# Kernel tuning notes

Hardware: AMD Instinct MI355X
Metric: run time of the kernel (lower is better)

## Reference

```python
import jax, jax.numpy as jnp
import numpy as np

# Grid / model constants (apt_original_dims = (B,H,W,T,BS,D))
B, H, W, T, BS, D = 8, 32, 32, 4, 3, 768
SMAX = 2  # apt_num_scales=2 -> patch sizes in {1, 2}


def _make_positions():
    """Tile each (H,W) grid per timestep with 2x2 blocks; exactly half the
    blocks become one coarse size-2 patch, the rest four size-1 patches.
    Returns int32 [B, P, 4] with rows (y, x, size, t); P identical per sample."""
    rng = np.random.default_rng(0)
    blocks = [(by, bx, t) for t in range(T) for by in range(H // SMAX) for bx in range(W // SMAX)]
    n_blocks = len(blocks)
    pos_all = []
    for b in range(B):
        coarse = rng.permutation(n_blocks) < n_blocks // 2
        plist = []
        for (by, bx, t), c in zip(blocks, coarse):
            y, x = by * SMAX, bx * SMAX
            if c:
                plist.append((y, x, SMAX, t))
            else:
                for dy in range(SMAX):
                    for dx in range(SMAX):
                        plist.append((y + dy, x + dx, 1, t))
        pos_all.append(plist)
    return np.asarray(pos_all, dtype=np.int32)  # [B, P, 4]


def setup_inputs() -> dict:
    key = jax.random.key(0)
    positions = jnp.asarray(_make_positions())            # [B, P, 4]
    P = positions.shape[1]                                # 2560
    modality_tokens = jax.random.normal(key, (B, P * BS, D), dtype=jnp.float32)
    return {"modality_tokens": modality_tokens, "positions": positions}


def reference(modality_tokens, positions):
    """Faithful jax version of split_and_expand_per_modality for the APT
    modality: scatter patch tokens to [B,H,W,T,BS,D], broadcasting coarse
    (size>1) tokens over the s x s grid cells they cover.
    Vectorized as: build a cell->patch-id map via one scatter, then gather."""
    Bn, P, _ = positions.shape
    y, x, size, t = positions[..., 0], positions[..., 1], positions[..., 2], positions[..., 3]

    # All offsets inside a max-size patch footprint: [SMAX*SMAX]
    dy, dx = jnp.meshgrid(jnp.arange(SMAX), jnp.arange(SMAX), indexing='ij')
    dy, dx = dy.reshape(-1), dx.reshape(-1)

    yy = y[:, :, None] + dy[None, None, :]                # [B, P, S2]
    xx = x[:, :, None] + dx[None, None, :]
    valid = (dy[None, None, :] < size[:, :, None]) & (dx[None, None, :] < size[:, :, None])

    flat = (yy * W + xx) * T + t[:, :, None]              # flat cell index
    flat = jnp.where(valid, flat, H * W * T)              # invalid -> dummy slot

    pid = jnp.broadcast_to(jnp.arange(P, dtype=jnp.int32)[None, :, None], flat.shape)
    b_idx = jnp.broadcast_to(jnp.arange(Bn)[:, None, None], flat.shape)

    id_map = jnp.full((Bn, H * W * T + 1), -1, dtype=jnp.int32)
    id_map = id_map.at[b_idx, flat].set(pid)              # cell -> covering patch id
    id_map = id_map[:, : H * W * T].reshape(Bn, H, W, T)

    tok = modality_tokens.reshape(Bn, P, BS, D)

    def gather_one(tok_b, idm_b):
        out = tok_b[jnp.maximum(idm_b, 0)]                # [H, W, T, BS, D]
        return jnp.where((idm_b >= 0)[..., None, None], out, jnp.zeros((), tok_b.dtype))

    return jax.vmap(gather_one)(tok, id_map)              # [B, H, W, T, BS, D]
```

## Files before the change

### kernel.cpp

```cpp
#include <hip/hip_runtime.h>


constexpr int H_ = 32;
constexpr int W_ = 32;
constexpr int T_ = 4;
constexpr int BS_ = 3;
constexpr int D_ = 768;
constexpr int CD  = BS_ * D_;
constexpr int CD4 = CD / 4;
constexpr int BLOCK = 192;
constexpr int BN_ = 8;
constexpr int CELLS = BN_ * H_ * W_ * T_;
constexpr int NXCD = 8;

typedef float f4 __attribute__((ext_vector_type(4)));

__global__ __launch_bounds__(256) void build_map_kernel(
    const int4* __restrict__ pos,
    int* __restrict__ map,
    int P)
{
    const int bp = blockIdx.x * 256 + threadIdx.x;
    if (bp >= BN_ * P) return;
    const int b = bp / P;
    const int4 q = pos[bp];
    const int y = q.x, x = q.y, size = q.z, t = q.w;
    const int c0 = (((b * H_ + y) * W_ + x) * T_) + t;
    map[c0] = bp;
    if (size == 2) {
        map[c0 + T_] = bp;
        map[c0 + W_ * T_] = bp;
        map[c0 + W_ * T_ + T_] = bp;
    }
}

__global__ __launch_bounds__(BLOCK) void apt_gather_kernel(
    const f4* __restrict__ tok,
    const int* __restrict__ map,
    f4* __restrict__ out)
{
    const int n = blockIdx.x;
    const int cell = (n & (NXCD - 1)) * (CELLS / NXCD) + (n >> 3);

    const int pid = map[cell];
    const f4* __restrict__ src = tok + (long)pid * CD4;
    f4* __restrict__ dst = out + (long)cell * CD4;

    const int tid = threadIdx.x;
    #pragma unroll
    for (int k = 0; k < CD4 / BLOCK; ++k) {
        const int i = tid + k * BLOCK;
        const f4 v = src[i];
        __builtin_nontemporal_store(v, &dst[i]);
    }
}

__global__ __launch_bounds__(BLOCK) void apt_scatter_kernel_nt(
    const f4* __restrict__ tok, const int4* __restrict__ pos,
    f4* __restrict__ out, int P)
{
    const int bp = blockIdx.x;
    const int b  = bp / P;
    const int4 q = pos[bp];
    const int y = q.x, x = q.y, size = q.z, t = q.w;
    const f4* __restrict__ src = tok + (long)bp * CD4;
    const long csy = (long)W_ * T_ * CD4;
    const long csx = (long)T_ * CD4;
    const long base0 = ((((long)b * H_ + y) * W_ + x) * T_ + t) * CD4;
    const int tid = threadIdx.x;
    if (size == 1) {
        f4* __restrict__ dst = out + base0;
        #pragma unroll
        for (int k = 0; k < CD4 / BLOCK; ++k) {
            const int i = tid + k * BLOCK;
            const f4 v = __builtin_nontemporal_load(&src[i]);
            __builtin_nontemporal_store(v, &dst[i]);
        }
    } else {
        f4* __restrict__ d00 = out + base0;
        f4* __restrict__ d01 = out + base0 + csx;
        f4* __restrict__ d10 = out + base0 + csy;
        f4* __restrict__ d11 = out + base0 + csy + csx;
        #pragma unroll
        for (int k = 0; k < CD4 / BLOCK; ++k) {
            const int i = tid + k * BLOCK;
            const f4 v = __builtin_nontemporal_load(&src[i]);
            __builtin_nontemporal_store(v, &d00[i]);
            __builtin_nontemporal_store(v, &d01[i]);
            __builtin_nontemporal_store(v, &d10[i]);
            __builtin_nontemporal_store(v, &d11[i]);
        }
    }
}

extern "C" void kernel_launch(void* const* d_in, const int* in_sizes, int n_in,
                              void* d_out, int out_size, void* d_ws, size_t ws_size,
                              hipStream_t stream) {
    const f4*   tok = (const f4*)d_in[0];
    const int4* pos = (const int4*)d_in[1];

    const int P = in_sizes[1] / (BN_ * 4);

    const size_t map_bytes = (size_t)CELLS * sizeof(int);
    if (d_ws != nullptr && ws_size >= map_bytes) {
        int* map = (int*)d_ws;
        const int total = BN_ * P;
        build_map_kernel<<<(total + 255) / 256, 256, 0, stream>>>(pos, map, P);
        apt_gather_kernel<<<CELLS, BLOCK, 0, stream>>>(tok, map, (f4*)d_out);
    } else {
        apt_scatter_kernel_nt<<<BN_ * P, BLOCK, 0, stream>>>(tok, pos, (f4*)d_out, P);
    }
}
```

Baseline: 427.0 us.

## Gather kernel: persistent waves each copying several consecutive cells

Replaces the one-block-per-cell gather, which launched 32768 blocks of 192 threads, with 1024 blocks of 4 waves. Each wave preloads the patch ids for 8 consecutive cells and copies each 9 KB row using 64 lanes with 9 float4s per lane. The aim is to cut block launch and scheduling overhead and give each thread more loads in flight, while keeping the per-XCD cell partitioning. The cost is fewer waves in flight overall, so latency hiding depends on per-lane memory-level parallelism.

```diff
diff --git a/kernel.cpp b/kernel.cpp
--- a/kernel.cpp
+++ b/kernel.cpp
@@ -8,10 +8,15 @@
 constexpr int D_ = 768;
 constexpr int CD  = BS_ * D_;
 constexpr int CD4 = CD / 4;
-constexpr int BLOCK = 192;
 constexpr int BN_ = 8;
 constexpr int CELLS = BN_ * H_ * W_ * T_;
 constexpr int NXCD = 8;
+
+constexpr int BLOCKS = 1024;
+constexpr int WAVES_PER_BLOCK = 4;
+constexpr int TOTAL_WAVES = BLOCKS * WAVES_PER_BLOCK;
+constexpr int CPW = CELLS / TOTAL_WAVES;
+constexpr int F4_PER_LANE = CD4 / 64;
 
 typedef float f4 __attribute__((ext_vector_type(4)));
 
@@ -34,28 +39,37 @@
     }
 }
 
-__global__ __launch_bounds__(BLOCK) void apt_gather_kernel(
+__global__ __launch_bounds__(256) void apt_gather2_kernel(
     const f4* __restrict__ tok,
     const int* __restrict__ map,
     f4* __restrict__ out)
 {
-    const int n = blockIdx.x;
-    const int cell = (n & (NXCD - 1)) * (CELLS / NXCD) + (n >> 3);
+    const int blk  = blockIdx.x;
+    const int xcd  = blk & (NXCD - 1);
+    const int jb   = blk >> 3;
+    const int wv   = threadIdx.x >> 6;
+    const int lane = threadIdx.x & 63;
 
-    const int pid = map[cell];
-    const f4* __restrict__ src = tok + (long)pid * CD4;
-    f4* __restrict__ dst = out + (long)cell * CD4;
+    const int cell0 = xcd * (CELLS / NXCD) + (jb * WAVES_PER_BLOCK + wv) * CPW;
 
-    const int tid = threadIdx.x;
+    int pid[CPW];
     #pragma unroll
-    for (int k = 0; k < CD4 / BLOCK; ++k) {
-        const int i = tid + k * BLOCK;
-        const f4 v = src[i];
-        __builtin_nontemporal_store(v, &dst[i]);
+    for (int c = 0; c < CPW; ++c) pid[c] = map[cell0 + c];
+
+    #pragma unroll
+    for (int c = 0; c < CPW; ++c) {
+        const f4* __restrict__ src = tok + (long)pid[c] * CD4 + lane;
+        f4* __restrict__ dst = out + (long)(cell0 + c) * CD4 + lane;
+        #pragma unroll
+        for (int k = 0; k < F4_PER_LANE; ++k) {
+            const f4 v = src[k * 64];
+            __builtin_nontemporal_store(v, &dst[k * 64]);
+        }
     }
 }
 
-__global__ __launch_bounds__(BLOCK) void apt_scatter_kernel_nt(
+constexpr int FBLOCK = 192;
+__global__ __launch_bounds__(FBLOCK) void apt_scatter_kernel_nt(
     const f4* __restrict__ tok, const int4* __restrict__ pos,
     f4* __restrict__ out, int P)
 {
@@ -71,8 +85,8 @@
     if (size == 1) {
         f4* __restrict__ dst = out + base0;
         #pragma unroll
-        for (int k = 0; k < CD4 / BLOCK; ++k) {
-            const int i = tid + k * BLOCK;
+        for (int k = 0; k < CD4 / FBLOCK; ++k) {
+            const int i = tid + k * FBLOCK;
             const f4 v = __builtin_nontemporal_load(&src[i]);
             __builtin_nontemporal_store(v, &dst[i]);
         }
@@ -82,8 +96,8 @@
         f4* __restrict__ d10 = out + base0 + csy;
         f4* __restrict__ d11 = out + base0 + csy + csx;
         #pragma unroll
-        for (int k = 0; k < CD4 / BLOCK; ++k) {
-            const int i = tid + k * BLOCK;
+        for (int k = 0; k < CD4 / FBLOCK; ++k) {
+            const int i = tid + k * FBLOCK;
             const f4 v = __builtin_nontemporal_load(&src[i]);
             __builtin_nontemporal_store(v, &d00[i]);
             __builtin_nontemporal_store(v, &d01[i]);
@@ -106,8 +120,8 @@
         int* map = (int*)d_ws;
         const int total = BN_ * P;
         build_map_kernel<<<(total + 255) / 256, 256, 0, stream>>>(pos, map, P);
-        apt_gather_kernel<<<CELLS, BLOCK, 0, stream>>>(tok, map, (f4*)d_out);
+        apt_gather2_kernel<<<BLOCKS, 256, 0, stream>>>(tok, map, (f4*)d_out);
     } else {
-        apt_scatter_kernel_nt<<<BN_ * P, BLOCK, 0, stream>>>(tok, pos, (f4*)d_out, P);
+        apt_scatter_kernel_nt<<<BN_ * P, FBLOCK, 0, stream>>>(tok, pos, (f4*)d_out, P);
     }
 }
```

After: 434.9 us. Within noise of the previous version (+1.8%).
